# Optimization experiments

Measured on AMD Instinct MI355X. Metric: run time of the kernel, lower is better.

The kernel has to match this reference:

```python
import jax, jax.numpy as jnp
import numpy as np

B, L, D, H, LAT, E, K, S, HID = 2, 1024, 1024, 16, 16, 8, 2, 2, 4096
HD = D // H  # 64 head dim


def _ln(x, g, b):
    m = x.mean(-1, keepdims=True)
    v = ((x - m) ** 2).mean(-1, keepdims=True)
    return (x - m) * jax.lax.rsqrt(v + 1e-5) * g + b


def _rope(t, cos, sin):
    # t: (B,H,L,HD); cos/sin: (1,1,L,HD//2); interleaved even/odd rotation
    te, to = t[..., ::2], t[..., 1::2]
    re = te * cos - to * sin
    ro = te * sin + to * cos
    return jnp.stack([re, ro], axis=-1).reshape(t.shape)


def setup_inputs() -> dict:
    key = jax.random.key(0)
    ks = iter(jax.random.split(key, 48))

    def w(shape, scale=0.02):
        return jax.random.normal(next(ks), shape, jnp.float32) * scale

    x = jax.random.normal(next(ks), (B, L, D), jnp.float32)
    pos = jnp.arange(L, dtype=jnp.float32)
    inv = 1.0 / (10000.0 ** (jnp.arange(0, HD, 2, dtype=jnp.float32) / HD))
    ang = pos[:, None] * inv[None, :]  # (L, HD//2)
    return dict(
        x=x, cos=jnp.cos(ang), sin=jnp.sin(ang),
        ln1_g=jnp.ones(D, jnp.float32), ln1_b=jnp.zeros(D, jnp.float32),
        Wq=w((D, D)), bq=jnp.zeros(D, jnp.float32),
        Wk=w((D, D)), bk=jnp.zeros(D, jnp.float32),
        Wv=w((D, D)), bv=jnp.zeros(D, jnp.float32),
        Wqc=w((HD, LAT)), bqc=jnp.zeros(LAT, jnp.float32),
        Wkc=w((HD, LAT)), bkc=jnp.zeros(LAT, jnp.float32),
        Wvc=w((HD, LAT)), bvc=jnp.zeros(LAT, jnp.float32),
        Wdc=w((LAT, HD)), bdc=jnp.zeros(HD, jnp.float32),
        Wo=w((D, D)), bo=jnp.zeros(D, jnp.float32),
        ln2_g=jnp.ones(D, jnp.float32), ln2_b=jnp.zeros(D, jnp.float32),
        Wr=w((D, E)), br=jnp.zeros(E, jnp.float32),
        We1=w((E, D, HID)), be1=jnp.zeros((E, HID), jnp.float32),
        We2=w((E, HID, D)), be2=jnp.zeros((E, D), jnp.float32),
        Ws1=w((S, D, HID)), bs1=jnp.zeros((S, HID), jnp.float32),
        Ws2=w((S, HID, D)), bs2=jnp.zeros((S, D), jnp.float32),
    )


def _fwd(x, cos, sin, ln1_g, ln1_b, Wq, bq, Wk, bk, Wv, bv, Wqc, bqc, Wkc, bkc,
         Wvc, bvc, Wdc, bdc, Wo, bo, ln2_g, ln2_b, Wr, br, We1, be1, We2, be2,
         Ws1, bs1, Ws2, bs2):
    Bx, Lx, Dm = x.shape
    # ---- Causal MLA attention ----
    h = _ln(x, ln1_g, ln1_b)
    q = (h @ Wq + bq).reshape(Bx, Lx, H, HD).transpose(0, 2, 1, 3)
    k = (h @ Wk + bk).reshape(Bx, Lx, H, HD).transpose(0, 2, 1, 3)
    v = (h @ Wv + bv).reshape(Bx, Lx, H, HD).transpose(0, 2, 1, 3)
    c = cos[:Lx][None, None]
    s = sin[:Lx][None, None]
    q = _rope(q, c, s)
    k = _rope(k, c, s)
    qc = q @ Wqc + bqc  # (B,H,L,LAT)
    kc = k @ Wkc + bkc
    vc = v @ Wvc + bvc
    scores = jnp.einsum('bhqc,bhkc->bhqk', qc, kc) / jnp.sqrt(jnp.float32(LAT))
    mask = jnp.triu(jnp.ones((Lx, Lx), bool), 1)
    scores = jnp.where(mask, -jnp.inf, scores)
    probs = jax.nn.softmax(scores, axis=-1)
    ao = jnp.einsum('bhqk,bhkc->bhqc', probs, vc) @ Wdc + bdc  # (B,H,L,HD)
    attn = ao.transpose(0, 2, 1, 3).reshape(Bx, Lx, Dm) @ Wo + bo
    x = x + attn
    # ---- MoE FFN ----
    h2 = _ln(x, ln2_g, ln2_b).reshape(-1, Dm)  # (N,D)
    # shared experts: always-on, averaged
    hs = jax.nn.gelu(jnp.einsum('nd,sdh->nsh', h2, Ws1) + bs1, approximate=False)
    shared = (jnp.einsum('nsh,shd->nsd', hs, Ws2) + bs2).mean(axis=1)
    # router -> top-k -> renormalized gates -> per-expert combine weights
    gates = h2 @ Wr + br
    vals, idx = jax.lax.top_k(gates, K)
    p = jax.nn.softmax(vals, axis=-1)  # (N,K)
    cw = (jax.nn.one_hot(idx, E, dtype=h2.dtype) * p[..., None]).sum(axis=1)  # (N,E)
    he = jax.nn.gelu(jnp.einsum('nd,edh->neh', h2, We1) + be1, approximate=False)
    oe = jnp.einsum('neh,ehd->ned', he, We2) + be2
    moe = jnp.einsum('ned,ne->nd', oe, cw)
    return x + (shared + moe).reshape(Bx, Lx, Dm)


def reference(x, cos, sin, ln1_g, ln1_b, Wq, bq, Wk, bk, Wv, bv, Wqc, bqc, Wkc,
              bkc, Wvc, bvc, Wdc, bdc, Wo, bo, ln2_g, ln2_b, Wr, br, We1, be1,
              We2, be2, Ws1, bs1, Ws2, bs2):
    return _fwd(x, cos, sin, ln1_g, ln1_b, Wq, bq, Wk, bk, Wv, bv, Wqc, bqc,
                Wkc, bkc, Wvc, bvc, Wdc, bdc, Wo, bo, ln2_g, ln2_b, Wr, br,
                We1, be1, We2, be2, Ws1, bs1, Ws2, bs2)
```

## Files before the change

### kernel.cpp

```cpp
#include <hip/hip_runtime.h>
#include <cstdint>

typedef unsigned short u16;
typedef __bf16 bf16x8 __attribute__((ext_vector_type(8)));
typedef float   f32x4 __attribute__((ext_vector_type(4)));
typedef u16     u16x8 __attribute__((ext_vector_type(8)));
typedef u16     u16x4 __attribute__((ext_vector_type(4)));

__device__ __forceinline__ u16 f2bf(float f) {
  union { float f; unsigned u; } v; v.f = f;
  unsigned r = (v.u + 0x7fffu + ((v.u >> 16) & 1u)) >> 16;
  return (u16)r;
}
__device__ __forceinline__ float bf2f(u16 h) {
  union { unsigned u; float f; } v; v.u = ((unsigned)h) << 16;
  return v.f;
}

__global__ void k_trans4(const float* __restrict__ w0, const float* __restrict__ w1,
                         const float* __restrict__ w2, const float* __restrict__ w3,
                         u16* __restrict__ dst) {
  __shared__ u16 t[32][33];
  int z = blockIdx.z;
  const float* src = z == 0 ? w0 : z == 1 ? w1 : z == 2 ? w2 : w3;
  u16* d = dst + (size_t)z * 1024 * 1024;
  int k0 = blockIdx.x * 32, n0 = blockIdx.y * 32;
  int tx = threadIdx.x, ty = threadIdx.y;
#pragma unroll
  for (int i = 0; i < 4; i++) {
    int r = ty + i * 8;
    t[r][tx] = f2bf(src[(size_t)(k0 + r) * 1024 + n0 + tx]);
  }
  __syncthreads();
#pragma unroll
  for (int i = 0; i < 4; i++) {
    int r = ty + i * 8;
    d[(size_t)(n0 + r) * 1024 + k0 + tx] = t[tx][r];
  }
}

__global__ void k_trans_exp(const float* __restrict__ pe, const float* __restrict__ ps,
                            u16* __restrict__ dst, int K, int N) {
  __shared__ u16 t[32][33];
  int z = blockIdx.z;
  size_t msz = (size_t)K * N;
  const float* src = z < 8 ? pe + (size_t)z * msz : ps + (size_t)(z - 8) * msz;
  u16* d = dst + (size_t)z * msz;
  int k0 = blockIdx.x * 32, n0 = blockIdx.y * 32;
  int tx = threadIdx.x, ty = threadIdx.y;
#pragma unroll
  for (int i = 0; i < 4; i++) {
    int r = ty + i * 8;
    t[r][tx] = f2bf(src[(size_t)(k0 + r) * N + n0 + tx]);
  }
  __syncthreads();
#pragma unroll
  for (int i = 0; i < 4; i++) {
    int r = ty + i * 8;
    d[(size_t)(n0 + r) * K + k0 + tx] = t[tx][r];
  }
}

__global__ void k_bias(const float* __restrict__ be1, const float* __restrict__ bs1,
                       const float* __restrict__ be2, const float* __restrict__ bs2,
                       float* __restrict__ b1a, float* __restrict__ b2a) {
  int i = blockIdx.x * 256 + threadIdx.x;
  if (i < 40960) b1a[i] = i < 32768 ? be1[i] : bs1[i - 32768];
  else {
    int j = i - 40960;
    if (j < 10240) b2a[j] = j < 8192 ? be2[j] : bs2[j - 8192];
  }
}

__global__ __launch_bounds__(256) void k_ln(const float* __restrict__ x,
                                            const float* __restrict__ g,
                                            const float* __restrict__ b,
                                            u16* __restrict__ outb,
                                            float* __restrict__ outf) {
  int row = blockIdx.x, tid = threadIdx.x;
  const float* xr = x + (size_t)row * 1024;
  float4 v = *(const float4*)(xr + tid * 4);
  float s1 = v.x + v.y + v.z + v.w;
  float s2 = v.x * v.x + v.y * v.y + v.z * v.z + v.w * v.w;
#pragma unroll
  for (int o = 32; o; o >>= 1) { s1 += __shfl_down(s1, o); s2 += __shfl_down(s2, o); }
  __shared__ float r1[4], r2[4], mv[2];
  int wave = tid >> 6;
  if ((tid & 63) == 0) { r1[wave] = s1; r2[wave] = s2; }
  __syncthreads();
  if (tid == 0) {
    float a = r1[0] + r1[1] + r1[2] + r1[3];
    float q = r2[0] + r2[1] + r2[2] + r2[3];
    float mean = a * (1.f / 1024.f);
    float var = q * (1.f / 1024.f) - mean * mean;
    mv[0] = mean; mv[1] = rsqrtf(var + 1e-5f);
  }
  __syncthreads();
  float mean = mv[0], inv = mv[1];
  int c = tid * 4;
  float4 gg = *(const float4*)(g + c);
  float4 bb = *(const float4*)(b + c);
  float o0 = (v.x - mean) * inv * gg.x + bb.x;
  float o1 = (v.y - mean) * inv * gg.y + bb.y;
  float o2 = (v.z - mean) * inv * gg.z + bb.z;
  float o3 = (v.w - mean) * inv * gg.w + bb.w;
  u16x4 h4 = { f2bf(o0), f2bf(o1), f2bf(o2), f2bf(o3) };
  *(u16x4*)(outb + (size_t)row * 1024 + c) = h4;
  if (outf) {
    float4 of = { o0, o1, o2, o3 };
    *(float4*)(outf + (size_t)row * 1024 + c) = of;
  }
}

#define TM 128
#define TN 128
#define BKK 64
#define LDKK 72

template<int EPI, bool GROUPED, bool GATHER>
__global__ __launch_bounds__(256, 2)
void k_gemm(const u16* __restrict__ A, const u16* __restrict__ Ball,
            const float* __restrict__ ball, void* __restrict__ outp,
            const float* __restrict__ res, int N, int K,
            const int* __restrict__ tmap, const int* __restrict__ stok) {
  int mtile = blockIdx.x, ntile = blockIdx.y;
  const u16* Bp = Ball;
  const float* bias = ball;
  if (GROUPED) {
    int e = tmap[mtile];
    if (e < 0) return;
    Bp = Ball + (size_t)e * N * K;
    bias = ball + (size_t)e * N;
  }
  __shared__ u16 As[TM][LDKK];
  __shared__ u16 Bs[TN][LDKK];
  __shared__ int rows[TM];
  int tid = threadIdx.x;
  if (GATHER) {
    if (tid < TM) rows[tid] = stok[mtile * TM + tid];
  }
  __syncthreads();
  int lane = tid & 63, wave = tid >> 6;
  int wm = (wave >> 1) * 64, wn = (wave & 1) * 64;
  int lm = lane & 15, lq = lane >> 4;
  f32x4 acc[4][4];
#pragma unroll
  for (int i = 0; i < 4; i++)
#pragma unroll
    for (int j = 0; j < 4; j++)
#pragma unroll
      for (int r = 0; r < 4; r++) acc[i][j][r] = 0.f;

  for (int k0 = 0; k0 < K; k0 += BKK) {
#pragma unroll
    for (int c = tid; c < TM * BKK / 8; c += 256) {
      int row = c >> 3, kc8 = (c & 7) << 3;
      size_t grow = GATHER ? (size_t)rows[row] : (size_t)mtile * TM + row;
      u16x8 vA = *(const u16x8*)(A + grow * K + k0 + kc8);
      *(u16x8*)&As[row][kc8] = vA;
      size_t gcol = (size_t)ntile * TN + row;
      u16x8 vB = *(const u16x8*)(Bp + gcol * K + k0 + kc8);
      *(u16x8*)&Bs[row][kc8] = vB;
    }
    __syncthreads();
#pragma unroll
    for (int ks = 0; ks < BKK; ks += 32) {
      bf16x8 af[4], bg[4];
#pragma unroll
      for (int i = 0; i < 4; i++) af[i] = *(const bf16x8*)&As[wm + i * 16 + lm][ks + lq * 8];
#pragma unroll
      for (int j = 0; j < 4; j++) bg[j] = *(const bf16x8*)&Bs[wn + j * 16 + lm][ks + lq * 8];
#pragma unroll
      for (int i = 0; i < 4; i++)
#pragma unroll
        for (int j = 0; j < 4; j++)
          acc[i][j] = __builtin_amdgcn_mfma_f32_16x16x32_bf16(af[i], bg[j], acc[i][j], 0, 0, 0);
    }
    __syncthreads();
  }

  size_t mbase = (size_t)mtile * TM;
#pragma unroll
  for (int i = 0; i < 4; i++) {
#pragma unroll
    for (int j = 0; j < 4; j++) {
      int rbase = wm + i * 16 + lq * 4;
      int col = ntile * TN + wn + j * 16 + lm;
      float bv = bias[col];
#pragma unroll
      for (int r = 0; r < 4; r++) {
        size_t grow = mbase + rbase + r;
        float v = acc[i][j][r] + bv;
        size_t off = grow * (size_t)N + col;
        if (EPI == 0) ((u16*)outp)[off] = f2bf(v);
        else if (EPI == 1) ((float*)outp)[off] = v + res[off];
        else if (EPI == 2) {
          float gl = 0.5f * v * (1.0f + erff(v * 0.70710678118f));
          ((u16*)outp)[off] = f2bf(gl);
        } else ((float*)outp)[off] = v;
      }
    }
  }
}

__global__ __launch_bounds__(256) void k_ropec(
    const u16* __restrict__ qb, const u16* __restrict__ kb, const u16* __restrict__ vb,
    const float* __restrict__ cosb, const float* __restrict__ sinb,
    const float* __restrict__ Wqc, const float* __restrict__ bqc,
    const float* __restrict__ Wkc, const float* __restrict__ bkc,
    const float* __restrict__ Wvc, const float* __restrict__ bvc,
    float* __restrict__ qc, float* __restrict__ kc, float* __restrict__ vc) {
  int z = blockIdx.z;
  int t = blockIdx.x * 256 + threadIdx.x;
  int r = t >> 4, j = t & 15;
  int bh = r >> 10, l = r & 1023;
  int b = bh >> 4, h = bh & 15;
  const u16* src = z == 0 ? qb : z == 1 ? kb : vb;
  const float* W = z == 0 ? Wqc : z == 1 ? Wkc : Wvc;
  const float* bi = z == 0 ? bqc : z == 1 ? bkc : bvc;
  float* dst = z == 0 ? qc : z == 1 ? kc : vc;
  size_t ib = ((size_t)(b * 1024 + l)) * 1024 + h * 64;
  float acc = bi[j];
  if (z < 2) {
#pragma unroll
    for (int i = 0; i < 32; i++) {
      float te = bf2f(src[ib + 2 * i]), to = bf2f(src[ib + 2 * i + 1]);
      float c = cosb[l * 32 + i], s = sinb[l * 32 + i];
      float re = te * c - to * s, ro = te * s + to * c;
      acc += re * W[(2 * i) * 16 + j] + ro * W[(2 * i + 1) * 16 + j];
    }
  } else {
#pragma unroll
    for (int d = 0; d < 64; d++) acc += bf2f(src[ib + d]) * W[d * 16 + j];
  }
  dst[((size_t)bh * 1024 + l) * 16 + j] = acc;
}

__global__ __launch_bounds__(256) void k_attn(
    const float* __restrict__ qc, const float* __restrict__ kc, const float* __restrict__ vc,
    const float* __restrict__ Wdc, const float* __restrict__ bdc, u16* __restrict__ ao) {
  __shared__ float kcs[128][16], vcs[128][16];
  int bh = blockIdx.y;
  int r = blockIdx.x * 256 + threadIdx.x;
  const float* qrow = qc + ((size_t)bh * 1024 + r) * 16;
  float q[16];
#pragma unroll
  for (int c = 0; c < 16; c += 4) {
    float4 v = *(const float4*)(qrow + c);
    q[c] = v.x; q[c + 1] = v.y; q[c + 2] = v.z; q[c + 3] = v.w;
  }
  float m = -1e30f, lsum = 0.f, acc[16];
#pragma unroll
  for (int c = 0; c < 16; c++) acc[c] = 0.f;
  int jmax = blockIdx.x * 256 + 255;
  for (int j0 = 0; j0 <= jmax; j0 += 128) {
    __syncthreads();
    for (int i = threadIdx.x; i < 512; i += 256) {
      int jr = i >> 2, c4 = (i & 3) << 2;
      size_t sb = ((size_t)bh * 1024 + j0 + jr) * 16 + c4;
      *(float4*)&kcs[jr][c4] = *(const float4*)(kc + sb);
      *(float4*)&vcs[jr][c4] = *(const float4*)(vc + sb);
    }
    __syncthreads();
    int jend = min(128, r - j0 + 1);
    for (int j = 0; j < jend; j++) {
      float s = 0.f;
#pragma unroll
      for (int c = 0; c < 16; c++) s += q[c] * kcs[j][c];
      s *= 0.25f;
      if (s > m) {
        float sc = __expf(m - s);
        m = s; lsum *= sc;
#pragma unroll
        for (int c = 0; c < 16; c++) acc[c] *= sc;
      }
      float p = __expf(s - m);
      lsum += p;
#pragma unroll
      for (int c = 0; c < 16; c++) acc[c] += p * vcs[j][c];
    }
  }
  float inv = 1.f / lsum;
#pragma unroll
  for (int c = 0; c < 16; c++) acc[c] *= inv;
  int b = bh >> 4, h = bh & 15;
  size_t ob = ((size_t)(b * 1024 + r)) * 1024 + h * 64;
#pragma unroll
  for (int d = 0; d < 64; d++) {
    float s = bdc[d];
#pragma unroll
    for (int c = 0; c < 16; c++) s += acc[c] * Wdc[c * 64 + d];
    ao[ob + d] = f2bf(s);
  }
}

__global__ __launch_bounds__(256) void k_gates(const float* __restrict__ h2f,
                                               const float* __restrict__ Wr,
                                               const float* __restrict__ br,
                                               int* __restrict__ eidx,
                                               float* __restrict__ ew) {
  int n = blockIdx.x, tid = threadIdx.x;
  int e = tid >> 5, i = tid & 31;
  const float* hr = h2f + (size_t)n * 1024;
  float s = 0.f;
  for (int d = i; d < 1024; d += 32) s += hr[d] * Wr[d * 8 + e];
#pragma unroll
  for (int o = 16; o; o >>= 1) s += __shfl_down(s, o, 32);
  __shared__ float gate[8];
  if (i == 0) gate[e] = s + br[e];
  __syncthreads();
  if (tid == 0) {
    float v0 = -1e30f, v1 = -1e30f; int i0 = 0, i1 = 0;
#pragma unroll
    for (int ee = 0; ee < 8; ee++) {
      float gv = gate[ee];
      if (gv > v0) { v1 = v0; i1 = i0; v0 = gv; i0 = ee; }
      else if (gv > v1) { v1 = gv; i1 = ee; }
    }
    float p0 = 1.f / (1.f + expf(v1 - v0));
    eidx[2 * n] = i0; eidx[2 * n + 1] = i1;
    ew[2 * n] = p0; ew[2 * n + 1] = 1.f - p0;
  }
}

__global__ void k_route(const int* __restrict__ eidx, int* __restrict__ stok,
                        int* __restrict__ posA, int* __restrict__ tmap) {
  __shared__ int cnt[8], base[8], cur[8];
  int tid = threadIdx.x;
  if (tid < 8) { cnt[tid] = 0; cur[tid] = 0; }
  __syncthreads();
  for (int a = tid; a < 4096; a += 256) atomicAdd(&cnt[eidx[a]], 1);
  __syncthreads();
  if (tid == 0) {
    for (int tt = 0; tt < 16; tt++) tmap[tt] = 8;
    for (int tt = 16; tt < 32; tt++) tmap[tt] = 9;
    int off = 4096, t = 32;
    for (int e = 0; e < 8; e++) {
      base[e] = off;
      int nt = (cnt[e] + 127) >> 7;
      for (int k = 0; k < nt; k++) tmap[t++] = e;
      off += nt * 128;
    }
    for (; t < 72; t++) tmap[t] = -1;
  }
  __syncthreads();
  for (int r = tid; r < 4096; r += 256) stok[r] = r & 2047;
  for (int r = 4096 + tid; r < 9216; r += 256) stok[r] = 0;
  __syncthreads();
  for (int a = tid; a < 4096; a += 256) {
    int e = eidx[a];
    int p = base[e] + atomicAdd(&cur[e], 1);
    stok[p] = a >> 1;
    posA[a] = p;
  }
}

__global__ __launch_bounds__(256) void k_combine(const float* __restrict__ x2,
                                                 const float* __restrict__ oe,
                                                 const int* __restrict__ posA,
                                                 const float* __restrict__ ew,
                                                 float* __restrict__ out) {
  int n = blockIdx.x, tid = threadIdx.x;
  int c = tid * 4;
  int p0 = posA[2 * n], p1 = posA[2 * n + 1];
  float w0 = ew[2 * n], w1 = ew[2 * n + 1];
  size_t bidx = (size_t)n * 1024 + c;
  float4 r = *(const float4*)(x2 + bidx);
  float4 s0 = *(const float4*)(oe + bidx);
  float4 s1 = *(const float4*)(oe + (size_t)(2048 + n) * 1024 + c);
  float4 m0 = *(const float4*)(oe + (size_t)p0 * 1024 + c);
  float4 m1 = *(const float4*)(oe + (size_t)p1 * 1024 + c);
  float4 o;
  o.x = r.x + 0.5f * (s0.x + s1.x) + w0 * m0.x + w1 * m1.x;
  o.y = r.y + 0.5f * (s0.y + s1.y) + w0 * m0.y + w1 * m1.y;
  o.z = r.z + 0.5f * (s0.z + s1.z) + w0 * m0.z + w1 * m1.z;
  o.w = r.w + 0.5f * (s0.w + s1.w) + w0 * m0.w + w1 * m1.w;
  *(float4*)(out + bidx) = o;
}

extern "C" void kernel_launch(void* const* d_in, const int* in_sizes, int n_in,
                              void* d_out, int out_size, void* d_ws, size_t ws_size,
                              hipStream_t stream) {
  const float* x    = (const float*)d_in[0];
  const float* cosb = (const float*)d_in[1];
  const float* sinb = (const float*)d_in[2];
  const float* ln1g = (const float*)d_in[3];
  const float* ln1b = (const float*)d_in[4];
  const float* Wq   = (const float*)d_in[5];
  const float* bq   = (const float*)d_in[6];
  const float* Wk   = (const float*)d_in[7];
  const float* bk   = (const float*)d_in[8];
  const float* Wv   = (const float*)d_in[9];
  const float* bv   = (const float*)d_in[10];
  const float* Wqc  = (const float*)d_in[11];
  const float* bqc  = (const float*)d_in[12];
  const float* Wkc  = (const float*)d_in[13];
  const float* bkc  = (const float*)d_in[14];
  const float* Wvc  = (const float*)d_in[15];
  const float* bvc  = (const float*)d_in[16];
  const float* Wdc  = (const float*)d_in[17];
  const float* bdc  = (const float*)d_in[18];
  const float* Wo   = (const float*)d_in[19];
  const float* bo   = (const float*)d_in[20];
  const float* ln2g = (const float*)d_in[21];
  const float* ln2b = (const float*)d_in[22];
  const float* Wr   = (const float*)d_in[23];
  const float* br   = (const float*)d_in[24];
  const float* We1  = (const float*)d_in[25];
  const float* be1  = (const float*)d_in[26];
  const float* We2  = (const float*)d_in[27];
  const float* be2  = (const float*)d_in[28];
  const float* Ws1  = (const float*)d_in[29];
  const float* bs1  = (const float*)d_in[30];
  const float* Ws2  = (const float*)d_in[31];
  const float* bs2  = (const float*)d_in[32];

  char* w = (char*)d_ws;
  size_t off = 0;
  auto alloc = [&](size_t bytes) -> void* {
    off = (off + 255) & ~(size_t)255;
    void* p = w + off;
    off += bytes;
    return p;
  };
  u16*   WT   = (u16*)alloc(4ull * 1024 * 1024 * 2);
  u16*   W1a  = (u16*)alloc(10ull * 4096 * 1024 * 2);
  u16*   W2a  = (u16*)alloc(10ull * 4096 * 1024 * 2);
  float* b1a  = (float*)alloc(10 * 4096 * 4);
  float* b2a  = (float*)alloc(10 * 1024 * 4);
  u16*   hbuf = (u16*)alloc(2048ull * 1024 * 2);
  u16*   qb   = (u16*)alloc(2048ull * 1024 * 2);
  u16*   kb   = (u16*)alloc(2048ull * 1024 * 2);
  u16*   vb   = (u16*)alloc(2048ull * 1024 * 2);
  float* qcb  = (float*)alloc(32768ull * 16 * 4);
  float* kcb  = (float*)alloc(32768ull * 16 * 4);
  float* vcb  = (float*)alloc(32768ull * 16 * 4);
  u16*   aob  = (u16*)alloc(2048ull * 1024 * 2);
  float* x2b  = (float*)alloc(2048ull * 1024 * 4);
  u16*   h2b  = (u16*)alloc(2048ull * 1024 * 2);
  float* h2f  = (float*)alloc(2048ull * 1024 * 4);
  int*   eidx = (int*)alloc(4096 * 4);
  float* ew   = (float*)alloc(4096 * 4);
  int*   posA = (int*)alloc(4096 * 4);
  int*   stok = (int*)alloc(9216 * 4);
  int*   tmap = (int*)alloc(72 * 4);
  u16*   heb  = (u16*)alloc(9216ull * 4096 * 2);
  float* oeb  = (float*)alloc(9216ull * 1024 * 4);
  (void)ws_size; (void)in_sizes; (void)n_in; (void)out_size;

  k_trans4   <<<dim3(32, 32, 4),  dim3(32, 8), 0, stream>>>(Wq, Wk, Wv, Wo, WT);
  k_trans_exp<<<dim3(32, 128, 10), dim3(32, 8), 0, stream>>>(We1, Ws1, W1a, 1024, 4096);
  k_trans_exp<<<dim3(128, 32, 10), dim3(32, 8), 0, stream>>>(We2, Ws2, W2a, 4096, 1024);
  k_bias     <<<200, 256, 0, stream>>>(be1, bs1, be2, bs2, b1a, b2a);

  k_ln<<<2048, 256, 0, stream>>>(x, ln1g, ln1b, hbuf, nullptr);
  k_gemm<0, false, false><<<dim3(16, 8), 256, 0, stream>>>(hbuf, WT,                bq, qb, nullptr, 1024, 1024, nullptr, nullptr);
  k_gemm<0, false, false><<<dim3(16, 8), 256, 0, stream>>>(hbuf, WT + 1048576,      bk, kb, nullptr, 1024, 1024, nullptr, nullptr);
  k_gemm<0, false, false><<<dim3(16, 8), 256, 0, stream>>>(hbuf, WT + 2097152,      bv, vb, nullptr, 1024, 1024, nullptr, nullptr);
  k_ropec<<<dim3(2048, 1, 3), 256, 0, stream>>>(qb, kb, vb, cosb, sinb,
                                                Wqc, bqc, Wkc, bkc, Wvc, bvc, qcb, kcb, vcb);
  k_attn<<<dim3(4, 32), 256, 0, stream>>>(qcb, kcb, vcb, Wdc, bdc, aob);
  k_gemm<1, false, false><<<dim3(16, 8), 256, 0, stream>>>(aob, WT + 3145728, bo, x2b, x, 1024, 1024, nullptr, nullptr);

  k_ln<<<2048, 256, 0, stream>>>(x2b, ln2g, ln2b, h2b, h2f);
  k_gates<<<2048, 256, 0, stream>>>(h2f, Wr, br, eidx, ew);
  k_route<<<1, 256, 0, stream>>>(eidx, stok, posA, tmap);
  k_gemm<2, true, true ><<<dim3(72, 32), 256, 0, stream>>>(h2b, W1a, b1a, heb, nullptr, 4096, 1024, tmap, stok);
  k_gemm<3, true, false><<<dim3(72, 8),  256, 0, stream>>>(heb, W2a, b2a, oeb, nullptr, 1024, 4096, tmap, nullptr);
  k_combine<<<2048, 256, 0, stream>>>(x2b, oeb, posA, ew, (float*)d_out);
}
```

Before: 1.214 ms.

## Fuse QKV GEMMs, use direct global-to-LDS loads, and alias workspace buffers

```diff
diff --git a/kernel.cpp b/kernel.cpp
--- a/kernel.cpp
+++ b/kernel.cpp
@@ -2,10 +2,18 @@
 #include <cstdint>
 
 typedef unsigned short u16;
+typedef unsigned int u32;
 typedef __bf16 bf16x8 __attribute__((ext_vector_type(8)));
 typedef float   f32x4 __attribute__((ext_vector_type(4)));
 typedef u16     u16x8 __attribute__((ext_vector_type(8)));
 typedef u16     u16x4 __attribute__((ext_vector_type(4)));
+
+#define AS1 __attribute__((address_space(1)))
+#define AS3 __attribute__((address_space(3)))
+
+__device__ __forceinline__ void gload_lds16(const void* g, void* l) {
+  __builtin_amdgcn_global_load_lds((const AS1 void*)g, (AS3 void*)l, 16, 0, 0);
+}
 
 __device__ __forceinline__ u16 f2bf(float f) {
   union { float f; unsigned u; } v; v.f = f;
@@ -63,13 +71,18 @@
 
 __global__ void k_bias(const float* __restrict__ be1, const float* __restrict__ bs1,
                        const float* __restrict__ be2, const float* __restrict__ bs2,
-                       float* __restrict__ b1a, float* __restrict__ b2a) {
+                       const float* __restrict__ bq, const float* __restrict__ bk,
+                       const float* __restrict__ bv,
+                       float* __restrict__ b1a, float* __restrict__ b2a,
+                       float* __restrict__ bqkv) {
   int i = blockIdx.x * 256 + threadIdx.x;
-  if (i < 40960) b1a[i] = i < 32768 ? be1[i] : bs1[i - 32768];
-  else {
-    int j = i - 40960;
-    if (j < 10240) b2a[j] = j < 8192 ? be2[j] : bs2[j - 8192];
-  }
+  if (i < 32768) b1a[i] = be1[i];
+  else if (i < 40960) b1a[i] = bs1[i - 32768];
+  else if (i < 49152) b2a[i - 40960] = be2[i - 40960];
+  else if (i < 51200) b2a[i - 40960] = bs2[i - 49152];
+  else if (i < 52224) bqkv[i - 51200] = bq[i - 51200];
+  else if (i < 53248) bqkv[i - 51200] = bk[i - 52224];
+  else if (i < 54272) bqkv[i - 51200] = bv[i - 53248];
 }
 
 __global__ __launch_bounds__(256) void k_ln(const float* __restrict__ x,
@@ -115,7 +128,6 @@
 #define TM 128
 #define TN 128
 #define BKK 64
-#define LDKK 72
 
 template<int EPI, bool GROUPED, bool GATHER>
 __global__ __launch_bounds__(256, 2)
@@ -132,15 +144,25 @@
     Bp = Ball + (size_t)e * N * K;
     bias = ball + (size_t)e * N;
   }
-  __shared__ u16 As[TM][LDKK];
-  __shared__ u16 Bs[TN][LDKK];
+  __shared__ u16 As[TM][BKK];
+  __shared__ u16 Bs[TN][BKK];
   __shared__ int rows[TM];
   int tid = threadIdx.x;
-  if (GATHER) {
-    if (tid < TM) rows[tid] = stok[mtile * TM + tid];
-  }
-  __syncthreads();
   int lane = tid & 63, wave = tid >> 6;
+  if (GATHER && tid < TM) rows[tid] = stok[mtile * TM + tid];
+  __syncthreads();
+
+  int srow = lane >> 3;
+  int scol = (lane & 7) << 3;
+  const u16* gA[4]; const u16* gB[4];
+#pragma unroll
+  for (int c = 0; c < 4; c++) {
+    int row = wave * 32 + c * 8 + srow;
+    size_t grow = GATHER ? (size_t)rows[row] : (size_t)mtile * TM + row;
+    gA[c] = A + grow * K + scol;
+    gB[c] = Bp + ((size_t)ntile * TN + row) * K + scol;
+  }
+
   int wm = (wave >> 1) * 64, wn = (wave & 1) * 64;
   int lm = lane & 15, lq = lane >> 4;
   f32x4 acc[4][4];
@@ -153,15 +175,11 @@
 
   for (int k0 = 0; k0 < K; k0 += BKK) {
 #pragma unroll
-    for (int c = tid; c < TM * BKK / 8; c += 256) {
-      int row = c >> 3, kc8 = (c & 7) << 3;
-      size_t grow = GATHER ? (size_t)rows[row] : (size_t)mtile * TM + row;
-      u16x8 vA = *(const u16x8*)(A + grow * K + k0 + kc8);
-      *(u16x8*)&As[row][kc8] = vA;
-      size_t gcol = (size_t)ntile * TN + row;
-      u16x8 vB = *(const u16x8*)(Bp + gcol * K + k0 + kc8);
-      *(u16x8*)&Bs[row][kc8] = vB;
-    }
+    for (int c = 0; c < 4; c++) {
+      gload_lds16(gA[c] + k0, &As[wave * 32 + c * 8][0]);
+      gload_lds16(gB[c] + k0, &Bs[wave * 32 + c * 8][0]);
+    }
+    __builtin_amdgcn_s_waitcnt(0);
     __syncthreads();
 #pragma unroll
     for (int ks = 0; ks < BKK; ks += 32) {
@@ -204,7 +222,7 @@
 }
 
 __global__ __launch_bounds__(256) void k_ropec(
-    const u16* __restrict__ qb, const u16* __restrict__ kb, const u16* __restrict__ vb,
+    const u16* __restrict__ qkvb,
     const float* __restrict__ cosb, const float* __restrict__ sinb,
     const float* __restrict__ Wqc, const float* __restrict__ bqc,
     const float* __restrict__ Wkc, const float* __restrict__ bkc,
@@ -215,23 +233,22 @@
   int r = t >> 4, j = t & 15;
   int bh = r >> 10, l = r & 1023;
   int b = bh >> 4, h = bh & 15;
-  const u16* src = z == 0 ? qb : z == 1 ? kb : vb;
   const float* W = z == 0 ? Wqc : z == 1 ? Wkc : Wvc;
   const float* bi = z == 0 ? bqc : z == 1 ? bkc : bvc;
   float* dst = z == 0 ? qc : z == 1 ? kc : vc;
-  size_t ib = ((size_t)(b * 1024 + l)) * 1024 + h * 64;
+  const u16* src = qkvb + (size_t)(b * 1024 + l) * 3072 + z * 1024 + h * 64;
   float acc = bi[j];
   if (z < 2) {
 #pragma unroll
     for (int i = 0; i < 32; i++) {
-      float te = bf2f(src[ib + 2 * i]), to = bf2f(src[ib + 2 * i + 1]);
+      float te = bf2f(src[2 * i]), to = bf2f(src[2 * i + 1]);
       float c = cosb[l * 32 + i], s = sinb[l * 32 + i];
       float re = te * c - to * s, ro = te * s + to * c;
       acc += re * W[(2 * i) * 16 + j] + ro * W[(2 * i + 1) * 16 + j];
     }
   } else {
 #pragma unroll
-    for (int d = 0; d < 64; d++) acc += bf2f(src[ib + d]) * W[d * 16 + j];
+    for (int d = 0; d < 64; d++) acc += bf2f(src[d]) * W[d * 16 + j];
   }
   dst[((size_t)bh * 1024 + l) * 16 + j] = acc;
 }
@@ -423,19 +440,11 @@
     off += bytes;
     return p;
   };
-  u16*   WT   = (u16*)alloc(4ull * 1024 * 1024 * 2);
   u16*   W1a  = (u16*)alloc(10ull * 4096 * 1024 * 2);
   u16*   W2a  = (u16*)alloc(10ull * 4096 * 1024 * 2);
   float* b1a  = (float*)alloc(10 * 4096 * 4);
   float* b2a  = (float*)alloc(10 * 1024 * 4);
-  u16*   hbuf = (u16*)alloc(2048ull * 1024 * 2);
-  u16*   qb   = (u16*)alloc(2048ull * 1024 * 2);
-  u16*   kb   = (u16*)alloc(2048ull * 1024 * 2);
-  u16*   vb   = (u16*)alloc(2048ull * 1024 * 2);
-  float* qcb  = (float*)alloc(32768ull * 16 * 4);
-  float* kcb  = (float*)alloc(32768ull * 16 * 4);
-  float* vcb  = (float*)alloc(32768ull * 16 * 4);
-  u16*   aob  = (u16*)alloc(2048ull * 1024 * 2);
+  float* bqkv = (float*)alloc(3072 * 4);
   float* x2b  = (float*)alloc(2048ull * 1024 * 4);
   u16*   h2b  = (u16*)alloc(2048ull * 1024 * 2);
   float* h2f  = (float*)alloc(2048ull * 1024 * 4);
@@ -444,20 +453,26 @@
   int*   posA = (int*)alloc(4096 * 4);
   int*   stok = (int*)alloc(9216 * 4);
   int*   tmap = (int*)alloc(72 * 4);
-  u16*   heb  = (u16*)alloc(9216ull * 4096 * 2);
   float* oeb  = (float*)alloc(9216ull * 1024 * 4);
+  char*  R    = (char*)alloc(9216ull * 4096 * 2);
+  u16*   heb  = (u16*)R;
+  u16*   WT   = (u16*)(R);
+  u16*   hbuf = (u16*)(R + 8388608);
+  u16*   qkvb = (u16*)(R + 8388608 + 4194304);
+  float* qcb  = (float*)(R + 25165824);
+  float* kcb  = (float*)(R + 27262976);
+  float* vcb  = (float*)(R + 29360128);
+  u16*   aob  = (u16*)(R + 31457280);
   (void)ws_size; (void)in_sizes; (void)n_in; (void)out_size;
 
   k_trans4   <<<dim3(32, 32, 4),  dim3(32, 8), 0, stream>>>(Wq, Wk, Wv, Wo, WT);
   k_trans_exp<<<dim3(32, 128, 10), dim3(32, 8), 0, stream>>>(We1, Ws1, W1a, 1024, 4096);
   k_trans_exp<<<dim3(128, 32, 10), dim3(32, 8), 0, stream>>>(We2, Ws2, W2a, 4096, 1024);
-  k_bias     <<<200, 256, 0, stream>>>(be1, bs1, be2, bs2, b1a, b2a);
+  k_bias     <<<212, 256, 0, stream>>>(be1, bs1, be2, bs2, bq, bk, bv, b1a, b2a, bqkv);
 
   k_ln<<<2048, 256, 0, stream>>>(x, ln1g, ln1b, hbuf, nullptr);
-  k_gemm<0, false, false><<<dim3(16, 8), 256, 0, stream>>>(hbuf, WT,                bq, qb, nullptr, 1024, 1024, nullptr, nullptr);
-  k_gemm<0, false, false><<<dim3(16, 8), 256, 0, stream>>>(hbuf, WT + 1048576,      bk, kb, nullptr, 1024, 1024, nullptr, nullptr);
-  k_gemm<0, false, false><<<dim3(16, 8), 256, 0, stream>>>(hbuf, WT + 2097152,      bv, vb, nullptr, 1024, 1024, nullptr, nullptr);
-  k_ropec<<<dim3(2048, 1, 3), 256, 0, stream>>>(qb, kb, vb, cosb, sinb,
+  k_gemm<0, false, false><<<dim3(16, 24), 256, 0, stream>>>(hbuf, WT, bqkv, qkvb, nullptr, 3072, 1024, nullptr, nullptr);
+  k_ropec<<<dim3(2048, 1, 3), 256, 0, stream>>>(qkvb, cosb, sinb,
                                                 Wqc, bqc, Wkc, bkc, Wvc, bvc, qcb, kcb, vcb);
   k_attn<<<dim3(4, 32), 256, 0, stream>>>(qcb, kcb, vcb, Wdc, bdc, aob);
   k_gemm<1, false, false><<<dim3(16, 8), 256, 0, stream>>>(aob, WT + 3145728, bo, x2b, x, 1024, 1024, nullptr, nullptr);
```

After: 1.014 ms. -16.4%, faster.
